# Kernel tuning notes

Measured on AMD Instinct MI355X. Metric: run time of the kernel, lower is better.

## Reference

```python
import jax, jax.numpy as jnp
import numpy as np

N = 32768   # nodes
E = 524288  # edges (avg degree 16)
F = 32      # num_features
H = 512     # hidden_channels
C = 10      # num_classes
G = 64      # graphs in batch


def setup_inputs() -> dict:
    key = jax.random.key(0)
    ks = jax.random.split(key, 16)
    s = 0.05  # weight init scale
    f32 = jnp.float32
    return {
        "x": jax.random.normal(ks[0], (N, F), f32),
        "edge_index": jax.random.randint(ks[1], (2, E), 0, N),
        "batch_index": jnp.sort(jax.random.randint(ks[2], (N,), 0, G)),
        # initial_conv: F -> H  (PyG GraphConv: lin_root on x, lin_rel on aggregated neighbors)
        "w_root0": jax.random.normal(ks[3], (F, H), f32) * s,
        "w_rel0": jax.random.normal(ks[4], (F, H), f32) * s,
        "b0": jnp.zeros((H,), f32),
        # conv1..conv4 stacked: H -> H
        "w_root": jax.random.normal(ks[5], (4, H, H), f32) * s,
        "w_rel": jax.random.normal(ks[6], (4, H, H), f32) * s,
        "b": jnp.zeros((4, H), f32),
        # MLP tail
        "lin1_w": jax.random.normal(ks[7], (2 * H, H), f32) * s,
        "lin1_b": jnp.zeros((H,), f32),
        "lin2_w": jax.random.normal(ks[8], (H, H), f32) * s,
        "lin2_b": jnp.zeros((H,), f32),
        "lin3_w": jax.random.normal(ks[9], (H, C), f32) * s,
        "lin3_b": jnp.zeros((C,), f32),
    }


def _graph_conv(h, src, dst, w_root, w_rel, bias):
    # out_i = h_i @ W_root + (sum_{j->i} h_j) @ W_rel + b   (PyG GraphConv, aggr='add')
    agg = jax.ops.segment_sum(h[src], dst, num_segments=N)
    return h @ w_root + agg @ w_rel + bias


def reference(x, edge_index, batch_index,
              w_root0, w_rel0, b0, w_root, w_rel, b,
              lin1_w, lin1_b, lin2_w, lin2_b, lin3_w, lin3_b):
    src, dst = edge_index[0], edge_index[1]
    h = jnp.tanh(_graph_conv(x, src, dst, w_root0, w_rel0, b0))
    for i in range(4):  # fixed small layer loop
        h = jnp.tanh(_graph_conv(h, src, dst, w_root[i], w_rel[i], b[i]))
    # global max + mean pool over graphs
    gmax = jax.ops.segment_max(h, batch_index, num_segments=G)
    gsum = jax.ops.segment_sum(h, batch_index, num_segments=G)
    cnt = jax.ops.segment_sum(jnp.ones((N,), h.dtype), batch_index, num_segments=G)
    gmean = gsum / jnp.maximum(cnt, 1.0)[:, None]
    g = jnp.concatenate([gmax, gmean], axis=1)  # [G, 2H]
    # dropout is identity at inference (training=False)
    g = jnp.tanh(g @ lin1_w + lin1_b)
    g = jnp.tanh(g @ lin2_w + lin2_b)
    logits = g @ lin3_w + lin3_b
    return jax.nn.log_softmax(logits, axis=1)
```

## Files before the change

### kernel.cpp

```cpp
#include <hip/hip_runtime.h>
#include <hip/hip_bf16.h>
#include <math.h>

#define NN 32768
#define EE 524288
#define FF 32
#define HH 512
#define GG 64
#define CC 10

typedef __attribute__((ext_vector_type(8))) short short8;
typedef __attribute__((ext_vector_type(4))) float floatx4;

__device__ __forceinline__ float bf16_to_f32(unsigned short u) {
    union { unsigned int u; float f; } v;
    v.u = ((unsigned int)u) << 16;
    return v.f;
}
__device__ __forceinline__ unsigned short f32_to_bf16(float f) {
    union { float f; unsigned int u; } v;
    v.f = f;
    unsigned int u = v.u;
    u += 0x7FFFu + ((u >> 16) & 1u);
    return (unsigned short)(u >> 16);
}
__device__ __forceinline__ float fast_tanh(float x) {
    float e = __expf(2.0f * x);
    return 1.0f - 2.0f * __builtin_amdgcn_rcpf(e + 1.0f);
}

__global__ void prep_all_kernel(const float* __restrict__ wr0, const float* __restrict__ wl0,
                                unsigned short* __restrict__ WT0,
                                const float* __restrict__ wroot, const float* __restrict__ wrel,
                                unsigned short* __restrict__ WTs,
                                const float* __restrict__ x, unsigned short* __restrict__ X0) {
    const int b = blockIdx.x;
    if (b < 128) {
        int t = b * 256 + threadIdx.x;
        int n = t >> 6, k = t & 63;
        float v = (k < 32) ? wr0[k * 512 + n] : wl0[(k - 32) * 512 + n];
        WT0[t] = f32_to_bf16(v);
    } else if (b < 8320) {
        int t = (b - 128) * 256 + threadIdx.x;
        int l = t >> 19;
        int r = t & 524287;
        int n = r >> 10, k = r & 1023;
        float v = (k < 512) ? wroot[(size_t)l * 262144 + k * 512 + n]
                            : wrel[(size_t)l * 262144 + (k - 512) * 512 + n];
        WTs[t] = f32_to_bf16(v);
    } else {
        int t = (b - 8320) * 256 + threadIdx.x;
        int i = t >> 5, c = t & 31;
        X0[(size_t)i * 64 + c] = f32_to_bf16(x[t]);
    }
}

__global__ void zero_i32(int* __restrict__ p, int n) {
    int i = blockIdx.x * blockDim.x + threadIdx.x;
    if (i < n) p[i] = 0;
}
__global__ void hist_kernel(const int* __restrict__ dst, int* __restrict__ counts) {
    int e = blockIdx.x * blockDim.x + threadIdx.x;
    if (e < EE) atomicAdd(&counts[dst[e]], 1);
}
__global__ __launch_bounds__(1024) void scan_kernel(const int* __restrict__ counts,
                                                    int* __restrict__ rowStart,
                                                    int* __restrict__ cursor) {
    __shared__ int part[1024];
    const int t = threadIdx.x;
    const int base = t * 32;
    int local[32];
    const int4* cp = (const int4*)(counts + base);
    int s = 0;
#pragma unroll
    for (int ii = 0; ii < 8; ++ii) {
        int4 v = cp[ii];
        local[ii * 4 + 0] = v.x; local[ii * 4 + 1] = v.y;
        local[ii * 4 + 2] = v.z; local[ii * 4 + 3] = v.w;
        s += v.x + v.y + v.z + v.w;
    }
    part[t] = s;
    __syncthreads();
    for (int off = 1; off < 1024; off <<= 1) {
        int v = (t >= off) ? part[t - off] : 0;
        __syncthreads();
        part[t] += v;
        __syncthreads();
    }
    int run = part[t] - s;
#pragma unroll
    for (int i = 0; i < 32; ++i) {
        rowStart[base + i] = run;
        cursor[base + i] = run;
        run += local[i];
    }
    if (t == 1023) rowStart[NN] = run;
}
__global__ void scatter_kernel(const int* __restrict__ src, const int* __restrict__ dst,
                               int* __restrict__ cursor, int* __restrict__ ssrc) {
    int e = blockIdx.x * blockDim.x + threadIdx.x;
    if (e < EE) {
        int p = atomicAdd(&cursor[dst[e]], 1);
        ssrc[p] = src[e];
    }
}

__device__ __forceinline__ void acc8(float* a, uint4 d) {
    a[0] += bf16_to_f32((unsigned short)(d.x & 0xFFFFu));
    a[1] += bf16_to_f32((unsigned short)(d.x >> 16));
    a[2] += bf16_to_f32((unsigned short)(d.y & 0xFFFFu));
    a[3] += bf16_to_f32((unsigned short)(d.y >> 16));
    a[4] += bf16_to_f32((unsigned short)(d.z & 0xFFFFu));
    a[5] += bf16_to_f32((unsigned short)(d.z >> 16));
    a[6] += bf16_to_f32((unsigned short)(d.w & 0xFFFFu));
    a[7] += bf16_to_f32((unsigned short)(d.w >> 16));
}

__global__ __launch_bounds__(256) void agg_kernel(const unsigned short* __restrict__ Xh, int ldh,
                                                  int cols, unsigned short* __restrict__ Xagg,
                                                  int ldagg, const int* __restrict__ rowStart,
                                                  const int* __restrict__ ssrc) {
    const int node = blockIdx.x * 4 + (threadIdx.x >> 6);
    const int lane = threadIdx.x & 63;
    const int chunks = cols >> 3;
    if (node >= NN || lane >= chunks) return;
    const int s = rowStart[node];
    const int e = rowStart[node + 1];
    float a[8] = {0.f, 0.f, 0.f, 0.f, 0.f, 0.f, 0.f, 0.f};
    const unsigned short* base = Xh + lane * 8;
    int i = s;
    for (; i + 4 <= e; i += 4) {
        int j0 = ssrc[i], j1 = ssrc[i + 1], j2 = ssrc[i + 2], j3 = ssrc[i + 3];
        uint4 d0 = *(const uint4*)(base + (size_t)j0 * ldh);
        uint4 d1 = *(const uint4*)(base + (size_t)j1 * ldh);
        uint4 d2 = *(const uint4*)(base + (size_t)j2 * ldh);
        uint4 d3 = *(const uint4*)(base + (size_t)j3 * ldh);
        acc8(a, d0); acc8(a, d1); acc8(a, d2); acc8(a, d3);
    }
    for (; i < e; ++i) {
        int j = ssrc[i];
        uint4 d = *(const uint4*)(base + (size_t)j * ldh);
        acc8(a, d);
    }
    unsigned short* out = Xagg + (size_t)node * ldagg + lane * 8;
#pragma unroll
    for (int c = 0; c < 8; ++c) out[c] = f32_to_bf16(a[c]);
}

__global__ __launch_bounds__(256) void agg_slice_kernel(const unsigned short* __restrict__ Xh,
                                                        unsigned short* __restrict__ Xagg,
                                                        const int* __restrict__ rowStart,
                                                        const int* __restrict__ ssrc) {
    const int slice = blockIdx.x & 7;
    const int nb = blockIdx.x >> 3;
    const int wv = threadIdx.x >> 6;
    const int lane = threadIdx.x & 63;
    const int ln = lane >> 3;
    const int lc = lane & 7;
    const int node = nb * 32 + wv * 8 + ln;
    const int colOff = slice * 64 + lc * 8;
    const int s = rowStart[node];
    const int e = rowStart[node + 1];
    float a[8] = {0.f, 0.f, 0.f, 0.f, 0.f, 0.f, 0.f, 0.f};
    const unsigned short* base = Xh + colOff;
    int i = s;
    for (; i + 8 <= e; i += 8) {
        int j0 = ssrc[i], j1 = ssrc[i + 1], j2 = ssrc[i + 2], j3 = ssrc[i + 3];
        int j4 = ssrc[i + 4], j5 = ssrc[i + 5], j6 = ssrc[i + 6], j7 = ssrc[i + 7];
        uint4 d0 = *(const uint4*)(base + (size_t)j0 * 1024);
        uint4 d1 = *(const uint4*)(base + (size_t)j1 * 1024);
        uint4 d2 = *(const uint4*)(base + (size_t)j2 * 1024);
        uint4 d3 = *(const uint4*)(base + (size_t)j3 * 1024);
        uint4 d4 = *(const uint4*)(base + (size_t)j4 * 1024);
        uint4 d5 = *(const uint4*)(base + (size_t)j5 * 1024);
        uint4 d6 = *(const uint4*)(base + (size_t)j6 * 1024);
        uint4 d7 = *(const uint4*)(base + (size_t)j7 * 1024);
        acc8(a, d0); acc8(a, d1); acc8(a, d2); acc8(a, d3);
        acc8(a, d4); acc8(a, d5); acc8(a, d6); acc8(a, d7);
    }
    for (; i < e; ++i) {
        int j = ssrc[i];
        uint4 d = *(const uint4*)(base + (size_t)j * 1024);
        acc8(a, d);
    }
    unsigned short* out = Xagg + (size_t)node * 1024 + colOff;
#pragma unroll
    for (int c = 0; c < 8; ++c) out[c] = f32_to_bf16(a[c]);
}

__global__ __launch_bounds__(256, 4) void gemm_bias_tanh(const unsigned short* __restrict__ Xin,
                                                         int ldin, int K,
                                                         const unsigned short* __restrict__ WT,
                                                         const float* __restrict__ bias,
                                                         unsigned short* __restrict__ Xout,
                                                         int ldout) {
    __shared__ __align__(16) unsigned short As[128 * 64];
    __shared__ __align__(16) unsigned short Bs[128 * 64];
    const int tid = threadIdx.x;
    const int lane = tid & 63;
    const int wave = tid >> 6;
    const int wm = wave >> 1, wn = wave & 1;
    const int bm = blockIdx.x, bn = blockIdx.y;

    floatx4 acc[4][4] = {};

    const int lrow = lane >> 3;
    const int schunk = (lane & 7) ^ (lrow & 7);
    const unsigned short* Abase = Xin + (size_t)(bm * 128) * ldin;
    const unsigned short* Bbase = WT + (size_t)(bn * 128) * K;
    const int m = lane & 15;
    const int quad = lane >> 4;

    for (int k0 = 0; k0 < K; k0 += 64) {
        __syncthreads();
#pragma unroll
        for (int q = 0; q < 4; ++q) {
            const int rr = q * 32 + wave * 8;
            const int row = rr + lrow;
            const unsigned short* sa = Abase + (size_t)row * ldin + (k0 + schunk * 8);
            const unsigned short* sb = Bbase + (size_t)row * K + (k0 + schunk * 8);
            __builtin_amdgcn_global_load_lds(
                (const __attribute__((address_space(1))) void*)sa,
                (__attribute__((address_space(3))) void*)(&As[rr * 64]), 16, 0, 0);
            __builtin_amdgcn_global_load_lds(
                (const __attribute__((address_space(1))) void*)sb,
                (__attribute__((address_space(3))) void*)(&Bs[rr * 64]), 16, 0, 0);
        }
        __syncthreads();
#pragma unroll
        for (int half = 0; half < 2; ++half) {
            short8 af[4], bfr[4];
#pragma unroll
            for (int t = 0; t < 4; ++t) {
                const int row = wm * 64 + t * 16 + m;
                const int chunk = (half * 4 + quad) ^ (row & 7);
                af[t] = *(const short8*)&As[row * 64 + chunk * 8];
            }
#pragma unroll
            for (int t = 0; t < 4; ++t) {
                const int row = wn * 64 + t * 16 + m;
                const int chunk = (half * 4 + quad) ^ (row & 7);
                bfr[t] = *(const short8*)&Bs[row * 64 + chunk * 8];
            }
#pragma unroll
            for (int mt = 0; mt < 4; ++mt)
#pragma unroll
                for (int nt = 0; nt < 4; ++nt)
                    acc[mt][nt] = __builtin_amdgcn_mfma_f32_16x16x32_bf16(af[mt], bfr[nt],
                                                                          acc[mt][nt], 0, 0, 0);
        }
    }

    const int row0 = bm * 128 + wm * 64;
    const int col0 = bn * 128 + wn * 64;
#pragma unroll
    for (int mt = 0; mt < 4; ++mt) {
#pragma unroll
        for (int nt = 0; nt < 4; ++nt) {
            const int col = col0 + nt * 16 + m;
            const float bv = bias[col];
#pragma unroll
            for (int r = 0; r < 4; ++r) {
                const int row = row0 + mt * 16 + quad * 4 + r;
                float v = fast_tanh(acc[mt][nt][r] + bv);
                Xout[(size_t)row * ldout + col] = f32_to_bf16(v);
            }
        }
    }
}

__global__ __launch_bounds__(256) void pool_partial(const unsigned short* __restrict__ h,
                                                    const int* __restrict__ batch,
                                                    float* __restrict__ part) {
    const int gi = blockIdx.x, rs = blockIdx.y, t = threadIdx.x;
    int lo = 0, hi = NN;
    while (lo < hi) { int mid = (lo + hi) >> 1; if (batch[mid] < gi) lo = mid + 1; else hi = mid; }
    const int start = lo;
    hi = NN;
    while (lo < hi) { int mid = (lo + hi) >> 1; if (batch[mid] < gi + 1) lo = mid + 1; else hi = mid; }
    const int end = lo;
    const int len = end - start;
    const int q = (len + 15) >> 4;
    int r0 = start + rs * q;
    int r1 = r0 + q; if (r1 > end) r1 = end; if (r0 > end) r0 = end;
    float mx0 = -INFINITY, mx1 = -INFINITY, s0 = 0.f, s1 = 0.f;
    int i = r0;
    for (; i + 2 <= r1; i += 2) {
        unsigned int d0 = *(const unsigned int*)(h + (size_t)i * 1024 + t * 2);
        unsigned int d1 = *(const unsigned int*)(h + (size_t)(i + 1) * 1024 + t * 2);
        float v0 = bf16_to_f32((unsigned short)(d0 & 0xFFFFu));
        float v1 = bf16_to_f32((unsigned short)(d0 >> 16));
        float w0 = bf16_to_f32((unsigned short)(d1 & 0xFFFFu));
        float w1 = bf16_to_f32((unsigned short)(d1 >> 16));
        mx0 = fmaxf(mx0, fmaxf(v0, w0)); mx1 = fmaxf(mx1, fmaxf(v1, w1));
        s0 += v0 + w0; s1 += v1 + w1;
    }
    for (; i < r1; ++i) {
        unsigned int d0 = *(const unsigned int*)(h + (size_t)i * 1024 + t * 2);
        float v0 = bf16_to_f32((unsigned short)(d0 & 0xFFFFu));
        float v1 = bf16_to_f32((unsigned short)(d0 >> 16));
        mx0 = fmaxf(mx0, v0); mx1 = fmaxf(mx1, v1);
        s0 += v0; s1 += v1;
    }
    float* p = part + ((size_t)gi * 16 + rs) * 1024;
    p[t * 2] = mx0; p[t * 2 + 1] = mx1;
    p[512 + t * 2] = s0; p[512 + t * 2 + 1] = s1;
}

__global__ __launch_bounds__(256) void pool_combine(const float* __restrict__ part,
                                                    const int* __restrict__ batch,
                                                    float* __restrict__ gT) {
    const int gi = blockIdx.x, t = threadIdx.x;
    int lo = 0, hi = NN;
    while (lo < hi) { int mid = (lo + hi) >> 1; if (batch[mid] < gi) lo = mid + 1; else hi = mid; }
    const int start = lo;
    hi = NN;
    while (lo < hi) { int mid = (lo + hi) >> 1; if (batch[mid] < gi + 1) lo = mid + 1; else hi = mid; }
    int cnt = lo - start; if (cnt < 1) cnt = 1;
    const float inv = 1.0f / (float)cnt;
    float mx0 = -INFINITY, mx1 = -INFINITY, s0 = 0.f, s1 = 0.f;
#pragma unroll
    for (int rs = 0; rs < 16; ++rs) {
        const float* p = part + ((size_t)gi * 16 + rs) * 1024;
        mx0 = fmaxf(mx0, p[t * 2]); mx1 = fmaxf(mx1, p[t * 2 + 1]);
        s0 += p[512 + t * 2]; s1 += p[512 + t * 2 + 1];
    }
    gT[(size_t)(2 * t) * 64 + gi]        = mx0;
    gT[(size_t)(2 * t + 1) * 64 + gi]    = mx1;
    gT[(size_t)(512 + 2 * t) * 64 + gi]  = s0 * inv;
    gT[(size_t)(512 + 2 * t + 1) * 64 + gi] = s1 * inv;
}

__global__ __launch_bounds__(256) void mlp_splitk(const float* __restrict__ ginT,
                                                  const float* __restrict__ W,
                                                  int Ndim,
                                                  float* __restrict__ partial) {
    __shared__ float gsT[64][68];
    __shared__ float Ws[64][68];
    const int t = threadIdx.x;
    const int wv = t >> 6, l = t & 63;
    const int nb = blockIdx.x, kb = blockIdx.y;
    const int n0 = nb * 64;
    const int gr = t >> 2;
    const int c4 = (t & 3) * 16;
    float acc[16] = {};
#pragma unroll
    for (int sub = 0; sub < 2; ++sub) {
        const int k0 = kb * 128 + sub * 64;
        __syncthreads();
        {
            const float4* gsrc = (const float4*)(ginT + (size_t)(k0 + gr) * 64 + c4);
            float4* gd = (float4*)&gsT[gr][c4];
            gd[0] = gsrc[0]; gd[1] = gsrc[1]; gd[2] = gsrc[2]; gd[3] = gsrc[3];
            const float4* wsrc = (const float4*)(W + (size_t)(k0 + gr) * Ndim + n0 + c4);
            float4* wd = (float4*)&Ws[gr][c4];
            wd[0] = wsrc[0]; wd[1] = wsrc[1]; wd[2] = wsrc[2]; wd[3] = wsrc[3];
        }
        __syncthreads();
#pragma unroll 4
        for (int kk = 0; kk < 64; ++kk) {
            const float wval = Ws[kk][l];
            const float4* gv = (const float4*)&gsT[kk][wv * 16];
            float4 g0 = gv[0], g1 = gv[1], g2 = gv[2], g3 = gv[3];
            acc[0]  = fmaf(g0.x, wval, acc[0]);  acc[1]  = fmaf(g0.y, wval, acc[1]);
            acc[2]  = fmaf(g0.z, wval, acc[2]);  acc[3]  = fmaf(g0.w, wval, acc[3]);
            acc[4]  = fmaf(g1.x, wval, acc[4]);  acc[5]  = fmaf(g1.y, wval, acc[5]);
            acc[6]  = fmaf(g1.z, wval, acc[6]);  acc[7]  = fmaf(g1.w, wval, acc[7]);
            acc[8]  = fmaf(g2.x, wval, acc[8]);  acc[9]  = fmaf(g2.y, wval, acc[9]);
            acc[10] = fmaf(g2.z, wval, acc[10]); acc[11] = fmaf(g2.w, wval, acc[11]);
            acc[12] = fmaf(g3.x, wval, acc[12]); acc[13] = fmaf(g3.y, wval, acc[13]);
            acc[14] = fmaf(g3.z, wval, acc[14]); acc[15] = fmaf(g3.w, wval, acc[15]);
        }
    }
    float* p = partial + ((size_t)kb * 64) * Ndim;
#pragma unroll
    for (int g = 0; g < 16; ++g)
        p[(size_t)(wv * 16 + g) * Ndim + n0 + l] = acc[g];
}

__global__ __launch_bounds__(256) void mlp_combine(const float* __restrict__ partial, int nparts,
                                                   const float* __restrict__ bias, int Ndim,
                                                   float* __restrict__ outN,
                                                   float* __restrict__ outT) {
    const int idx = blockIdx.x * 256 + threadIdx.x;
    if (idx >= 64 * Ndim) return;
    const int g = idx / Ndim, n = idx - g * Ndim;
    float s = bias[n];
    for (int kb = 0; kb < nparts; ++kb)
        s += partial[((size_t)kb * 64 + g) * Ndim + n];
    const float v = fast_tanh(s);
    if (outN) outN[(size_t)g * Ndim + n] = v;
    if (outT) outT[(size_t)n * 64 + g] = v;
}

__global__ __launch_bounds__(64) void head_kernel(const float* __restrict__ g2,
                                                  const float* __restrict__ W,
                                                  const float* __restrict__ b,
                                                  float* __restrict__ out) {
    const int gi = blockIdx.x, t = threadIdx.x;
    const float4* gp = (const float4*)(g2 + (size_t)gi * HH + t * 8);
    float4 ga = gp[0], gb = gp[1];
    float gv[8] = {ga.x, ga.y, ga.z, ga.w, gb.x, gb.y, gb.z, gb.w};
    float logits[CC];
#pragma unroll
    for (int c = 0; c < CC; ++c) {
        float p = 0.f;
#pragma unroll
        for (int j = 0; j < 8; ++j)
            p = fmaf(gv[j], W[(t * 8 + j) * CC + c], p);
#pragma unroll
        for (int off = 32; off > 0; off >>= 1)
            p += __shfl_xor(p, off, 64);
        logits[c] = p + b[c];
    }
    if (t == 0) {
        float mx = logits[0];
#pragma unroll
        for (int c = 1; c < CC; ++c) mx = fmaxf(mx, logits[c]);
        float s = 0.f;
#pragma unroll
        for (int c = 0; c < CC; ++c) s += expf(logits[c] - mx);
        float lse = mx + logf(s);
#pragma unroll
        for (int c = 0; c < CC; ++c) out[(size_t)gi * CC + c] = logits[c] - lse;
    }
}

extern "C" void kernel_launch(void* const* d_in, const int* in_sizes, int n_in,
                              void* d_out, int out_size, void* d_ws, size_t ws_size,
                              hipStream_t stream) {
    const float* x       = (const float*)d_in[0];
    const int*   ei      = (const int*)d_in[1];
    const int*   batch   = (const int*)d_in[2];
    const float* w_root0 = (const float*)d_in[3];
    const float* w_rel0  = (const float*)d_in[4];
    const float* b0      = (const float*)d_in[5];
    const float* w_root  = (const float*)d_in[6];
    const float* w_rel   = (const float*)d_in[7];
    const float* bvec    = (const float*)d_in[8];
    const float* lin1_w  = (const float*)d_in[9];
    const float* lin1_b  = (const float*)d_in[10];
    const float* lin2_w  = (const float*)d_in[11];
    const float* lin2_b  = (const float*)d_in[12];
    const float* lin3_w  = (const float*)d_in[13];
    const float* lin3_b  = (const float*)d_in[14];
    float* out = (float*)d_out;

    char* w = (char*)d_ws;
    size_t off = 0;
    auto alloc = [&](size_t bytes) -> char* {
        char* p = w + off;
        off += (bytes + 255) & ~(size_t)255;
        return p;
    };
    unsigned short* Xa  = (unsigned short*)alloc((size_t)NN * 1024 * 2);
    unsigned short* Xb  = (unsigned short*)alloc((size_t)NN * 1024 * 2);
    unsigned short* X0  = (unsigned short*)alloc((size_t)NN * 64 * 2);
    unsigned short* WT0 = (unsigned short*)alloc(512 * 64 * 2);
    unsigned short* WTs = (unsigned short*)alloc((size_t)4 * 512 * 1024 * 2);
    int* counts   = (int*)alloc((size_t)NN * 4);
    int* rowStart = (int*)alloc((size_t)(NN + 1) * 4);
    int* cursor   = (int*)alloc((size_t)NN * 4);
    int* ssrc     = (int*)alloc((size_t)EE * 4);
    float* gbufT  = (float*)alloc((size_t)1024 * 64 * 4);
    float* g1T    = (float*)alloc((size_t)512 * 64 * 4);
    float* g2buf  = (float*)alloc((size_t)GG * 512 * 4);
    float* mlpPart = (float*)alloc((size_t)8 * 64 * 512 * 4);
    float* part   = (float*)X0;

    const int* esrc = ei;
    const int* edst = ei + EE;

    prep_all_kernel<<<12416, 256, 0, stream>>>(w_root0, w_rel0, WT0, w_root, w_rel, WTs, x, X0);
    zero_i32<<<128, 256, 0, stream>>>(counts, NN);
    hist_kernel<<<2048, 256, 0, stream>>>(edst, counts);
    scan_kernel<<<1, 1024, 0, stream>>>(counts, rowStart, cursor);
    scatter_kernel<<<2048, 256, 0, stream>>>(esrc, edst, cursor, ssrc);

    agg_kernel<<<8192, 256, 0, stream>>>(X0, 64, 32, X0 + 32, 64, rowStart, ssrc);
    gemm_bias_tanh<<<dim3(256, 4), 256, 0, stream>>>(X0, 64, 64, WT0, b0, Xa, 1024);

    agg_slice_kernel<<<8192, 256, 0, stream>>>(Xa, Xa + 512, rowStart, ssrc);
    gemm_bias_tanh<<<dim3(256, 4), 256, 0, stream>>>(Xa, 1024, 1024, WTs + 0 * 524288, bvec + 0, Xb, 1024);
    agg_slice_kernel<<<8192, 256, 0, stream>>>(Xb, Xb + 512, rowStart, ssrc);
    gemm_bias_tanh<<<dim3(256, 4), 256, 0, stream>>>(Xb, 1024, 1024, WTs + 1 * 524288, bvec + 512, Xa, 1024);
    agg_slice_kernel<<<8192, 256, 0, stream>>>(Xa, Xa + 512, rowStart, ssrc);
    gemm_bias_tanh<<<dim3(256, 4), 256, 0, stream>>>(Xa, 1024, 1024, WTs + 2 * 524288, bvec + 1024, Xb, 1024);
    agg_slice_kernel<<<8192, 256, 0, stream>>>(Xb, Xb + 512, rowStart, ssrc);
    gemm_bias_tanh<<<dim3(256, 4), 256, 0, stream>>>(Xb, 1024, 1024, WTs + 3 * 524288, bvec + 1536, Xa, 1024);

    pool_partial<<<dim3(GG, 16), 256, 0, stream>>>(Xa, batch, part);
    pool_combine<<<GG, 256, 0, stream>>>(part, batch, gbufT);
    mlp_splitk<<<dim3(8, 8), 256, 0, stream>>>(gbufT, lin1_w, 512, mlpPart);
    mlp_combine<<<128, 256, 0, stream>>>(mlpPart, 8, lin1_b, 512, nullptr, g1T);
    mlp_splitk<<<dim3(8, 4), 256, 0, stream>>>(g1T, lin2_w, 512, mlpPart);
    mlp_combine<<<128, 256, 0, stream>>>(mlpPart, 4, lin2_b, 512, g2buf, nullptr);
    head_kernel<<<GG, 64, 0, stream>>>(g2buf, lin3_w, lin3_b, out);
}
```

Baseline: 668.4 us.

## Sort nodes by degree for aggregation and fuse pooling with MLP tail

Adds a counting-sort permutation of nodes by in-degree so each aggregation wave handles nodes of similar degree, which is meant to reduce lane divergence in the gather loop. Fuses the pool combine with the lin1 GEMV, and lin2 with the classifier head, replacing the split-K MLP kernels and cutting the tail from seven launches to three. Also halves the pool partial splits. This adds three small preprocessing kernels. The permuted node order may scatter writes and hurt locality, and the new MLP kernels do long serial K loops.

```diff
diff --git a/kernel.cpp b/kernel.cpp
--- a/kernel.cpp
+++ b/kernel.cpp
@@ -104,6 +104,37 @@
         ssrc[p] = src[e];
     }
 }
+__global__ void deg_hist_kernel(const int* __restrict__ counts, int* __restrict__ degHist) {
+    int i = blockIdx.x * blockDim.x + threadIdx.x;
+    if (i < NN) {
+        int d = counts[i]; if (d > 255) d = 255;
+        atomicAdd(&degHist[d], 1);
+    }
+}
+__global__ __launch_bounds__(256) void deg_scan_kernel(const int* __restrict__ degHist,
+                                                       int* __restrict__ degCursor) {
+    __shared__ int sh[256];
+    const int t = threadIdx.x;
+    int own = degHist[t];
+    sh[t] = own;
+    __syncthreads();
+    for (int off = 1; off < 256; off <<= 1) {
+        int v = (t >= off) ? sh[t - off] : 0;
+        __syncthreads();
+        sh[t] += v;
+        __syncthreads();
+    }
+    degCursor[t] = sh[t] - own;
+}
+__global__ void deg_scatter_kernel(const int* __restrict__ counts, int* __restrict__ degCursor,
+                                   int* __restrict__ perm) {
+    int i = blockIdx.x * blockDim.x + threadIdx.x;
+    if (i < NN) {
+        int d = counts[i]; if (d > 255) d = 255;
+        int p = atomicAdd(&degCursor[d], 1);
+        perm[p] = i;
+    }
+}
 
 __device__ __forceinline__ void acc8(float* a, uint4 d) {
     a[0] += bf16_to_f32((unsigned short)(d.x & 0xFFFFu));
@@ -150,14 +181,15 @@
 __global__ __launch_bounds__(256) void agg_slice_kernel(const unsigned short* __restrict__ Xh,
                                                         unsigned short* __restrict__ Xagg,
                                                         const int* __restrict__ rowStart,
-                                                        const int* __restrict__ ssrc) {
+                                                        const int* __restrict__ ssrc,
+                                                        const int* __restrict__ perm) {
     const int slice = blockIdx.x & 7;
     const int nb = blockIdx.x >> 3;
     const int wv = threadIdx.x >> 6;
     const int lane = threadIdx.x & 63;
     const int ln = lane >> 3;
     const int lc = lane & 7;
-    const int node = nb * 32 + wv * 8 + ln;
+    const int node = perm[nb * 32 + wv * 8 + ln];
     const int colOff = slice * 64 + lc * 8;
     const int s = rowStart[node];
     const int e = rowStart[node + 1];
@@ -280,7 +312,7 @@
     while (lo < hi) { int mid = (lo + hi) >> 1; if (batch[mid] < gi + 1) lo = mid + 1; else hi = mid; }
     const int end = lo;
     const int len = end - start;
-    const int q = (len + 15) >> 4;
+    const int q = (len + 7) >> 3;
     int r0 = start + rs * q;
     int r1 = r0 + q; if (r1 > end) r1 = end; if (r0 > end) r0 = end;
     float mx0 = -INFINITY, mx1 = -INFINITY, s0 = 0.f, s1 = 0.f;
@@ -302,15 +334,21 @@
         mx0 = fmaxf(mx0, v0); mx1 = fmaxf(mx1, v1);
         s0 += v0; s1 += v1;
     }
-    float* p = part + ((size_t)gi * 16 + rs) * 1024;
+    float* p = part + ((size_t)gi * 8 + rs) * 1024;
     p[t * 2] = mx0; p[t * 2 + 1] = mx1;
     p[512 + t * 2] = s0; p[512 + t * 2 + 1] = s1;
 }
 
-__global__ __launch_bounds__(256) void pool_combine(const float* __restrict__ part,
-                                                    const int* __restrict__ batch,
-                                                    float* __restrict__ gT) {
-    const int gi = blockIdx.x, t = threadIdx.x;
+__global__ __launch_bounds__(256) void pool_lin1_kernel(const float* __restrict__ part,
+                                                        const int* __restrict__ batch,
+                                                        const float* __restrict__ W1,
+                                                        const float* __restrict__ b1,
+                                                        float* __restrict__ g1) {
+    __shared__ float gbuf[1024];
+    __shared__ float red[128];
+    const int b = blockIdx.x;
+    const int gi = b >> 2, q = b & 3;
+    const int t = threadIdx.x;
     int lo = 0, hi = NN;
     while (lo < hi) { int mid = (lo + hi) >> 1; if (batch[mid] < gi) lo = mid + 1; else hi = mid; }
     const int start = lo;
@@ -318,101 +356,59 @@
     while (lo < hi) { int mid = (lo + hi) >> 1; if (batch[mid] < gi + 1) lo = mid + 1; else hi = mid; }
     int cnt = lo - start; if (cnt < 1) cnt = 1;
     const float inv = 1.0f / (float)cnt;
-    float mx0 = -INFINITY, mx1 = -INFINITY, s0 = 0.f, s1 = 0.f;
-#pragma unroll
-    for (int rs = 0; rs < 16; ++rs) {
-        const float* p = part + ((size_t)gi * 16 + rs) * 1024;
-        mx0 = fmaxf(mx0, p[t * 2]); mx1 = fmaxf(mx1, p[t * 2 + 1]);
-        s0 += p[512 + t * 2]; s1 += p[512 + t * 2 + 1];
-    }
-    gT[(size_t)(2 * t) * 64 + gi]        = mx0;
-    gT[(size_t)(2 * t + 1) * 64 + gi]    = mx1;
-    gT[(size_t)(512 + 2 * t) * 64 + gi]  = s0 * inv;
-    gT[(size_t)(512 + 2 * t + 1) * 64 + gi] = s1 * inv;
-}
-
-__global__ __launch_bounds__(256) void mlp_splitk(const float* __restrict__ ginT,
-                                                  const float* __restrict__ W,
-                                                  int Ndim,
-                                                  float* __restrict__ partial) {
-    __shared__ float gsT[64][68];
-    __shared__ float Ws[64][68];
-    const int t = threadIdx.x;
-    const int wv = t >> 6, l = t & 63;
-    const int nb = blockIdx.x, kb = blockIdx.y;
-    const int n0 = nb * 64;
-    const int gr = t >> 2;
-    const int c4 = (t & 3) * 16;
-    float acc[16] = {};
-#pragma unroll
-    for (int sub = 0; sub < 2; ++sub) {
-        const int k0 = kb * 128 + sub * 64;
-        __syncthreads();
-        {
-            const float4* gsrc = (const float4*)(ginT + (size_t)(k0 + gr) * 64 + c4);
-            float4* gd = (float4*)&gsT[gr][c4];
-            gd[0] = gsrc[0]; gd[1] = gsrc[1]; gd[2] = gsrc[2]; gd[3] = gsrc[3];
-            const float4* wsrc = (const float4*)(W + (size_t)(k0 + gr) * Ndim + n0 + c4);
-            float4* wd = (float4*)&Ws[gr][c4];
-            wd[0] = wsrc[0]; wd[1] = wsrc[1]; wd[2] = wsrc[2]; wd[3] = wsrc[3];
+    for (int f = t; f < 512; f += 256) {
+        float mx = -INFINITY, sm = 0.f;
+#pragma unroll
+        for (int rs = 0; rs < 8; ++rs) {
+            const float* p = part + ((size_t)(gi * 8 + rs)) * 1024;
+            mx = fmaxf(mx, p[f]);
+            sm += p[512 + f];
         }
-        __syncthreads();
+        gbuf[f] = mx;
+        gbuf[512 + f] = sm * inv;
+    }
+    __syncthreads();
+    const int n = q * 128 + (t & 127);
+    const int k0 = (t >> 7) * 512;
+    float acc = 0.f;
+#pragma unroll 8
+    for (int k = 0; k < 512; ++k)
+        acc = fmaf(gbuf[k0 + k], W1[(size_t)(k0 + k) * 512 + n], acc);
+    if (t >= 128) red[t - 128] = acc;
+    __syncthreads();
+    if (t < 128)
+        g1[(size_t)gi * 512 + n] = fast_tanh(acc + red[t] + b1[n]);
+}
+
+__global__ __launch_bounds__(256) void lin2_head_kernel(const float* __restrict__ g1,
+                                                        const float* __restrict__ W2,
+                                                        const float* __restrict__ b2,
+                                                        const float* __restrict__ W3,
+                                                        const float* __restrict__ b3,
+                                                        float* __restrict__ out) {
+    __shared__ float g1s[512];
+    __shared__ float g2s[512];
+    __shared__ float logits[CC];
+    const int gi = blockIdx.x, t = threadIdx.x;
+    for (int f = t; f < 512; f += 256) g1s[f] = g1[(size_t)gi * 512 + f];
+    __syncthreads();
+    float a0 = 0.f, a1 = 0.f;
+    const int n0 = t, n1 = t + 256;
 #pragma unroll 4
-        for (int kk = 0; kk < 64; ++kk) {
-            const float wval = Ws[kk][l];
-            const float4* gv = (const float4*)&gsT[kk][wv * 16];
-            float4 g0 = gv[0], g1 = gv[1], g2 = gv[2], g3 = gv[3];
-            acc[0]  = fmaf(g0.x, wval, acc[0]);  acc[1]  = fmaf(g0.y, wval, acc[1]);
-            acc[2]  = fmaf(g0.z, wval, acc[2]);  acc[3]  = fmaf(g0.w, wval, acc[3]);
-            acc[4]  = fmaf(g1.x, wval, acc[4]);  acc[5]  = fmaf(g1.y, wval, acc[5]);
-            acc[6]  = fmaf(g1.z, wval, acc[6]);  acc[7]  = fmaf(g1.w, wval, acc[7]);
-            acc[8]  = fmaf(g2.x, wval, acc[8]);  acc[9]  = fmaf(g2.y, wval, acc[9]);
-            acc[10] = fmaf(g2.z, wval, acc[10]); acc[11] = fmaf(g2.w, wval, acc[11]);
-            acc[12] = fmaf(g3.x, wval, acc[12]); acc[13] = fmaf(g3.y, wval, acc[13]);
-            acc[14] = fmaf(g3.z, wval, acc[14]); acc[15] = fmaf(g3.w, wval, acc[15]);
-        }
-    }
-    float* p = partial + ((size_t)kb * 64) * Ndim;
-#pragma unroll
-    for (int g = 0; g < 16; ++g)
-        p[(size_t)(wv * 16 + g) * Ndim + n0 + l] = acc[g];
-}
-
-__global__ __launch_bounds__(256) void mlp_combine(const float* __restrict__ partial, int nparts,
-                                                   const float* __restrict__ bias, int Ndim,
-                                                   float* __restrict__ outN,
-                                                   float* __restrict__ outT) {
-    const int idx = blockIdx.x * 256 + threadIdx.x;
-    if (idx >= 64 * Ndim) return;
-    const int g = idx / Ndim, n = idx - g * Ndim;
-    float s = bias[n];
-    for (int kb = 0; kb < nparts; ++kb)
-        s += partial[((size_t)kb * 64 + g) * Ndim + n];
-    const float v = fast_tanh(s);
-    if (outN) outN[(size_t)g * Ndim + n] = v;
-    if (outT) outT[(size_t)n * 64 + g] = v;
-}
-
-__global__ __launch_bounds__(64) void head_kernel(const float* __restrict__ g2,
-                                                  const float* __restrict__ W,
-                                                  const float* __restrict__ b,
-                                                  float* __restrict__ out) {
-    const int gi = blockIdx.x, t = threadIdx.x;
-    const float4* gp = (const float4*)(g2 + (size_t)gi * HH + t * 8);
-    float4 ga = gp[0], gb = gp[1];
-    float gv[8] = {ga.x, ga.y, ga.z, ga.w, gb.x, gb.y, gb.z, gb.w};
-    float logits[CC];
-#pragma unroll
-    for (int c = 0; c < CC; ++c) {
-        float p = 0.f;
-#pragma unroll
-        for (int j = 0; j < 8; ++j)
-            p = fmaf(gv[j], W[(t * 8 + j) * CC + c], p);
-#pragma unroll
-        for (int off = 32; off > 0; off >>= 1)
-            p += __shfl_xor(p, off, 64);
-        logits[c] = p + b[c];
-    }
+    for (int k = 0; k < 512; ++k) {
+        float g = g1s[k];
+        a0 = fmaf(g, W2[(size_t)k * 512 + n0], a0);
+        a1 = fmaf(g, W2[(size_t)k * 512 + n1], a1);
+    }
+    g2s[n0] = fast_tanh(a0 + b2[n0]);
+    g2s[n1] = fast_tanh(a1 + b2[n1]);
+    __syncthreads();
+    if (t < CC) {
+        float a = b3[t];
+        for (int k = 0; k < 512; ++k) a = fmaf(g2s[k], W3[k * CC + t], a);
+        logits[t] = a;
+    }
+    __syncthreads();
     if (t == 0) {
         float mx = logits[0];
 #pragma unroll
@@ -459,41 +455,40 @@
     unsigned short* WT0 = (unsigned short*)alloc(512 * 64 * 2);
     unsigned short* WTs = (unsigned short*)alloc((size_t)4 * 512 * 1024 * 2);
     int* counts   = (int*)alloc((size_t)NN * 4);
+    int* degHist  = (int*)alloc(256 * 4);
+    int* degCursor= (int*)alloc(256 * 4);
     int* rowStart = (int*)alloc((size_t)(NN + 1) * 4);
     int* cursor   = (int*)alloc((size_t)NN * 4);
     int* ssrc     = (int*)alloc((size_t)EE * 4);
-    float* gbufT  = (float*)alloc((size_t)1024 * 64 * 4);
-    float* g1T    = (float*)alloc((size_t)512 * 64 * 4);
-    float* g2buf  = (float*)alloc((size_t)GG * 512 * 4);
-    float* mlpPart = (float*)alloc((size_t)8 * 64 * 512 * 4);
+    int* perm     = (int*)alloc((size_t)NN * 4);
+    float* g1     = (float*)alloc((size_t)GG * 512 * 4);
     float* part   = (float*)X0;
 
     const int* esrc = ei;
     const int* edst = ei + EE;
 
     prep_all_kernel<<<12416, 256, 0, stream>>>(w_root0, w_rel0, WT0, w_root, w_rel, WTs, x, X0);
-    zero_i32<<<128, 256, 0, stream>>>(counts, NN);
+    zero_i32<<<130, 256, 0, stream>>>(counts, NN + 256);
     hist_kernel<<<2048, 256, 0, stream>>>(edst, counts);
     scan_kernel<<<1, 1024, 0, stream>>>(counts, rowStart, cursor);
     scatter_kernel<<<2048, 256, 0, stream>>>(esrc, edst, cursor, ssrc);
+    deg_hist_kernel<<<128, 256, 0, stream>>>(counts, degHist);
+    deg_scan_kernel<<<1, 256, 0, stream>>>(degHist, degCursor);
+    deg_scatter_kernel<<<128, 256, 0, stream>>>(counts, degCursor, perm);
 
     agg_kernel<<<8192, 256, 0, stream>>>(X0, 64, 32, X0 + 32, 64, rowStart, ssrc);
     gemm_bias_tanh<<<dim3(256, 4), 256, 0, stream>>>(X0, 64, 64, WT0, b0, Xa, 1024);
 
-    agg_slice_kernel<<<8192, 256, 0, stream>>>(Xa, Xa + 512, rowStart, ssrc);
+    agg_slice_kernel<<<8192, 256, 0, stream>>>(Xa, Xa + 512, rowStart, ssrc, perm);
     gemm_bias_tanh<<<dim3(256, 4), 256, 0, stream>>>(Xa, 1024, 1024, WTs + 0 * 524288, bvec + 0, Xb, 1024);
-    agg_slice_kernel<<<8192, 256, 0, stream>>>(Xb, Xb + 512, rowStart, ssrc);
+    agg_slice_kernel<<<8192, 256, 0, stream>>>(Xb, Xb + 512, rowStart, ssrc, perm);
     gemm_bias_tanh<<<dim3(256, 4), 256, 0, stream>>>(Xb, 1024, 1024, WTs + 1 * 524288, bvec + 512, Xa, 1024);
-    agg_slice_kernel<<<8192, 256, 0, stream>>>(Xa, Xa + 512, rowStart, ssrc);
+    agg_slice_kernel<<<8192, 256, 0, stream>>>(Xa, Xa + 512, rowStart, ssrc, perm);
     gemm_bias_tanh<<<dim3(256, 4), 256, 0, stream>>>(Xa, 1024, 1024, WTs + 2 * 524288, bvec + 1024, Xb, 1024);
-    agg_slice_kernel<<<8192, 256, 0, stream>>>(Xb, Xb + 512, rowStart, ssrc);
+    agg_slice_kernel<<<8192, 256, 0, stream>>>(Xb, Xb + 512, rowStart, ssrc, perm);
     gemm_bias_tanh<<<dim3(256, 4), 256, 0, stream>>>(Xb, 1024, 1024, WTs + 3 * 524288, bvec + 1536, Xa, 1024);
 
-    pool_partial<<<dim3(GG, 16), 256, 0, stream>>>(Xa, batch, part);
-    pool_combine<<<GG, 256, 0, stream>>>(part, batch, gbufT);
-    mlp_splitk<<<dim3(8, 8), 256, 0, stream>>>(gbufT, lin1_w, 512, mlpPart);
-    mlp_combine<<<128, 256, 0, stream>>>(mlpPart, 8, lin1_b, 512, nullptr, g1T);
-    mlp_splitk<<<dim3(8, 4), 256, 0, stream>>>(g1T, lin2_w, 512, mlpPart);
-    mlp_combine<<<128, 256, 0, stream>>>(mlpPart, 4, lin2_b, 512, g2buf, nullptr);
-    head_kernel<<<GG, 64, 0, stream>>>(g2buf, lin3_w, lin3_b, out);
-}
+    pool_partial<<<dim3(GG, 8), 256, 0, stream>>>(Xa, batch, part);
+    pool_lin1_kernel<<<256, 256, 0, stream>>>(part, batch, lin1_w, lin1_b, g1);
+    lin2_head_kernel<<<GG, 256, 0, stream>>>(g1, lin2_w, lin2_b, lin3_w, lin3_b, out);
+}
```

Result: slower. 867.1 us (+29.7%).
